# Kernel optimization log

Hardware: AMD Instinct MI355X
Metric: run time of the kernel (lower is better)

The kernel has to match this reference:

```python
import jax, jax.numpy as jnp
import numpy as np

EMBED_DIM = 1024
NUM_HEADS = 16
HEAD_DIM = EMBED_DIM // NUM_HEADS  # used only for the softmax scale


def setup_inputs() -> dict:
    key = jax.random.key(0)
    k_x, k_wqkv, k_bqkv, k_wo, k_bo = jax.random.split(key, 5)
    bound_qkv = 1.0 / np.sqrt(EMBED_DIM)
    return {
        "x": jax.random.normal(k_x, (4, 2048, EMBED_DIM), dtype=jnp.float32),
        "W_qkv": jax.random.uniform(k_wqkv, (EMBED_DIM, 3 * EMBED_DIM), jnp.float32, -bound_qkv, bound_qkv),
        "b_qkv": jax.random.uniform(k_bqkv, (3 * EMBED_DIM,), jnp.float32, -bound_qkv, bound_qkv),
        "W_out": jax.random.uniform(k_wo, (EMBED_DIM, EMBED_DIM), jnp.float32, -bound_qkv, bound_qkv),
        "b_out": jax.random.uniform(k_bo, (EMBED_DIM,), jnp.float32, -bound_qkv, bound_qkv),
    }


def reference(x, W_qkv, b_qkv, W_out, b_out):
    # fused QKV projection: [B,S,3E]
    qkv = jnp.einsum("bse,ef->bsf", x, W_qkv) + b_qkv
    q, k, v = jnp.split(qkv, 3, axis=-1)  # each [B,S,E]
    scale = 1.0 / jnp.sqrt(jnp.float32(HEAD_DIM))
    # NOTE: no head reshape — attention over full embed_dim, scale uses head_dim
    scores = jnp.einsum("bqe,bke->bqk", q, k) * scale  # [B,S,S]
    attn = jax.nn.softmax(scores, axis=-1)
    context = jnp.einsum("bqk,bke->bqe", attn, v)  # [B,S,E]
    return jnp.einsum("bse,ef->bsf", context, W_out) + b_out
```

## Files before the change

### kernel.cpp

```cpp
#include <hip/hip_runtime.h>

typedef unsigned short u16;
typedef __bf16   bf16x8 __attribute__((ext_vector_type(8)));
typedef float    f32x4  __attribute__((ext_vector_type(4)));
typedef unsigned short u16x4 __attribute__((ext_vector_type(4)));

__device__ inline float bf2f(u16 u) { return __uint_as_float(((unsigned int)u) << 16); }
__device__ inline u16 f2bf(float f) {
    unsigned int u = __float_as_uint(f);
    u += 0x7FFF + ((u >> 16) & 1);
    return (u16)(u >> 16);
}

__device__ inline void gl2lds16(const u16* g, u16* l) {
    __builtin_amdgcn_global_load_lds(
        (const __attribute__((address_space(1))) void*)g,
        (__attribute__((address_space(3))) void*)l, 16, 0, 0);
}

__global__ __launch_bounds__(256)
void sniff_zero(const u16* __restrict__ x, int* __restrict__ flag,
                float* __restrict__ sums) {
    sums[blockIdx.x * 256 + threadIdx.x] = 0.0f;
    if (blockIdx.x == 0 && threadIdx.x < 64) {
        const int lane = threadIdx.x;
        const unsigned idx = lane * 131072u + 65536u;
        const u16 u = x[idx];
        const int e = (u >> 7) & 0xFF;
        const unsigned long long b = __ballot(e >= 100 && e <= 140);
        if (lane == 0) flag[0] = (__popcll(b) >= 48) ? 0 : 1;
    }
}

__global__ __launch_bounds__(256)
void convx_biases(const void* __restrict__ x, u16* __restrict__ xbf,
                  const void* __restrict__ b1, const void* __restrict__ b2,
                  u16* __restrict__ o1, u16* __restrict__ o2,
                  const int* __restrict__ flagp) {
    const int f = *flagp;
    if (blockIdx.x < 8192) {
        const long i = ((long)blockIdx.x * 256 + threadIdx.x) * 4;
        if (f) {
            f32x4 v = *(const f32x4*)((const float*)x + i);
            u16x4 o; o[0] = f2bf(v[0]); o[1] = f2bf(v[1]); o[2] = f2bf(v[2]); o[3] = f2bf(v[3]);
            *(u16x4*)(xbf + i) = o;
        } else {
            *(u16x4*)(xbf + i) = *(const u16x4*)((const u16*)x + i);
        }
    } else {
        const int i = (blockIdx.x - 8192) * 256 + threadIdx.x;
        if (i < 3072) o1[i] = f ? f2bf(((const float*)b1)[i]) : ((const u16*)b1)[i];
        else { const int j = i - 3072;
               o2[j] = f ? f2bf(((const float*)b2)[j]) : ((const u16*)b2)[j]; }
    }
}

__global__ __launch_bounds__(256)
void transpose_w(const void* __restrict__ Wqkv, u16* __restrict__ WqkvT,
                 const void* __restrict__ Wout, u16* __restrict__ WoutT,
                 const int* __restrict__ flagp)
{
    const void* in; u16* out; long inStride, outStride;
    if (blockIdx.z == 0) { in = Wqkv; out = WqkvT; inStride = 3072; outStride = 1024; }
    else { if (blockIdx.x >= 32) return;
           in = Wout; out = WoutT; inStride = 1024; outStride = 1024; }
    __shared__ u16 t[32][36];
    const int isF32 = *flagp;
    const int tid = threadIdx.x;
    const long r0 = (long)blockIdx.y * 32;
    const long c0 = (long)blockIdx.x * 32;
    const int r  = tid >> 3;
    const int c4 = (tid & 7) * 4;
    const long base = (r0 + r) * inStride + c0 + c4;
    u16x4 v;
    if (isF32) {
        f32x4 f = *(const f32x4*)((const float*)in + base);
        v[0] = f2bf(f[0]); v[1] = f2bf(f[1]); v[2] = f2bf(f[2]); v[3] = f2bf(f[3]);
    } else {
        v = *(const u16x4*)((const u16*)in + base);
    }
    t[r][c4 + 0] = v[0]; t[r][c4 + 1] = v[1]; t[r][c4 + 2] = v[2]; t[r][c4 + 3] = v[3];
    __syncthreads();
    u16x4 o;
    o[0] = t[c4 + 0][r]; o[1] = t[c4 + 1][r]; o[2] = t[c4 + 2][r]; o[3] = t[c4 + 3][r];
    *(u16x4*)&out[(c0 + r) * outStride + r0 + c4] = o;
}

template <int GM, int GN, int WM, int WN, int EPI, int OUT_MODE, bool HAS_BIAS>
__global__ __launch_bounds__(256, 4)
void gemm_t(const u16* __restrict__ A, const u16* __restrict__ Bt,
            void* __restrict__ Cv, const u16* __restrict__ bias,
            int K, long lda, long ldb, long ldc,
            long aBatch, long bBatch, long cBatch, float scale,
            const int* __restrict__ flagp, float* __restrict__ sums)
{
    constexpr int BM = GM * WM * 16;
    constexpr int BN = GN * WN * 16;
    constexpr int IA = BM / 32;
    constexpr int IB = BN / 32;
    __shared__ __align__(16) u16 As[BM * 64];
    __shared__ __align__(16) u16 Bs[BN * 64];

    const int outF32 = (OUT_MODE == 2) ? *flagp : OUT_MODE;

    const int tid  = threadIdx.x;
    const int lane = tid & 63;
    const int wave = tid >> 6;
    const long m0 = (long)blockIdx.y * BM;
    const long n0 = (long)blockIdx.x * BN;
    const long bz = blockIdx.z;

    const int sr  = tid >> 3;
    const int qg0 = (tid & 7) ^ (sr & 7);
    const u16* pa[IA];
    const u16* pb[IB];
    u16* la[IA];
    u16* lb[IB];
#pragma unroll
    for (int i = 0; i < IA; ++i) {
        pa[i] = A + bz * aBatch + (m0 + i * 32 + sr) * lda + qg0 * 8;
        la[i] = As + (i * 256 + wave * 64) * 8;
    }
#pragma unroll
    for (int i = 0; i < IB; ++i) {
        pb[i] = Bt + bz * bBatch + (n0 + i * 32 + sr) * ldb + qg0 * 8;
        lb[i] = Bs + (i * 256 + wave * 64) * 8;
    }

    const int wm = (wave / GN) * (WM * 16);
    const int wn = (wave % GN) * (WN * 16);
    const int lr = lane & 15;
    const int hk = lane >> 4;

    int aoff[WM][2], boff[WN][2];
#pragma unroll
    for (int i = 0; i < WM; ++i) {
        const int row = wm + i * 16 + lr, r7 = row & 7;
        aoff[i][0] = row * 64 + ((hk     ^ r7) * 8);
        aoff[i][1] = row * 64 + (((4+hk) ^ r7) * 8);
    }
#pragma unroll
    for (int j = 0; j < WN; ++j) {
        const int row = wn + j * 16 + lr, r7 = row & 7;
        boff[j][0] = row * 64 + ((hk     ^ r7) * 8);
        boff[j][1] = row * 64 + (((4+hk) ^ r7) * 8);
    }

    f32x4 acc[WM][WN] = {};

    for (int kt = 0; kt < K; kt += 64) {
#pragma unroll
        for (int i = 0; i < IA; ++i) { gl2lds16(pa[i], la[i]); pa[i] += 64; }
#pragma unroll
        for (int i = 0; i < IB; ++i) { gl2lds16(pb[i], lb[i]); pb[i] += 64; }
        __syncthreads();

#pragma unroll
        for (int ks = 0; ks < 2; ++ks) {
            bf16x8 af[WM], bf[WN];
#pragma unroll
            for (int i = 0; i < WM; ++i) af[i] = *(const bf16x8*)&As[aoff[i][ks]];
#pragma unroll
            for (int j = 0; j < WN; ++j) bf[j] = *(const bf16x8*)&Bs[boff[j][ks]];
#pragma unroll
            for (int i = 0; i < WM; ++i)
#pragma unroll
                for (int j = 0; j < WN; ++j)
                    acc[i][j] = __builtin_amdgcn_mfma_f32_16x16x32_bf16(af[i], bf[j], acc[i][j], 0, 0, 0);
        }
        __syncthreads();
    }

    if (EPI == 1) {
#pragma unroll
        for (int i = 0; i < WM; ++i) {
#pragma unroll
            for (int r = 0; r < 4; ++r) {
                const long row = m0 + wm + i*16 + hk*4 + r;
                float s = 0.0f;
#pragma unroll
                for (int j = 0; j < WN; ++j) {
                    const long c = n0 + wn + j*16 + lr;
                    const float e = __expf(acc[i][j][r] * scale);
                    ((u16*)Cv)[bz * cBatch + row * ldc + c] = f2bf(e);
                    s += e;
                }
                s += __shfl_xor(s, 1); s += __shfl_xor(s, 2);
                s += __shfl_xor(s, 4); s += __shfl_xor(s, 8);
                if (lr == 0) atomicAdd(&sums[bz * 2048 + row], s);
            }
        }
    } else {
        float inv[WM][4];
        if (EPI == 2) {
#pragma unroll
            for (int i = 0; i < WM; ++i)
#pragma unroll
                for (int r = 0; r < 4; ++r)
                    inv[i][r] = 1.0f / sums[bz * 2048 + m0 + wm + i*16 + hk*4 + r];
        }
#pragma unroll
        for (int j = 0; j < WN; ++j) {
            const long c = n0 + wn + j*16 + lr;
            const float bj = HAS_BIAS ? bf2f(bias[c]) : 0.0f;
#pragma unroll
            for (int i = 0; i < WM; ++i) {
                const long rbase = m0 + wm + i*16 + hk * 4;
#pragma unroll
                for (int r = 0; r < 4; ++r) {
                    float v = (EPI == 2) ? acc[i][j][r] * inv[i][r] + bj
                                         : acc[i][j][r] * scale + bj;
                    const long ci = bz * cBatch + (rbase + r) * ldc + c;
                    if (outF32) ((float*)Cv)[ci] = v;
                    else        ((u16*)Cv)[ci]   = f2bf(v);
                }
            }
        }
    }
}

extern "C" void kernel_launch(void* const* d_in, const int* in_sizes, int n_in,
                              void* d_out, int out_size, void* d_ws, size_t ws_size,
                              hipStream_t stream)
{
    const void* x    = d_in[0];
    const void* Wqkv = d_in[1];
    const void* bqkv = d_in[2];
    const void* Wout = d_in[3];
    const void* bout = d_in[4];
    char* ws = (char*)d_ws;

    u16*   xbf   = (u16*)(ws);
    u16*   WqkvT = (u16*)(ws + 16777216);
    u16*   P     = (u16*)(ws);
    u16*   QKV   = (u16*)(ws + 33554432);
    u16*   VWT   = (u16*)(ws + 83886080);
    u16*   WoutT = (u16*)(ws + 100663296);
    u16*   bqkvc = (u16*)(ws + 102760448);
    u16*   boutc = (u16*)(ws + 102766592);
    int*   flag  = (int*)(ws + 102768640);
    float* sums  = (float*)(ws + 102772736);

    dim3 blk(256);

    sniff_zero<<<32, blk, 0, stream>>>((const u16*)x, flag, sums);
    convx_biases<<<8208, blk, 0, stream>>>(x, xbf, bqkv, bout, bqkvc, boutc, flag);
    transpose_w<<<dim3(96, 32, 2), blk, 0, stream>>>(Wqkv, WqkvT, Wout, WoutT, flag);

    gemm_t<2, 2, 4, 4, 0, 0, true><<<dim3(24, 64, 1), blk, 0, stream>>>(
        xbf, WqkvT, QKV, bqkvc, 1024, 1024L, 1024L, 3072L,
        0L, 0L, 0L, 1.0f, nullptr, nullptr);

    gemm_t<2, 2, 4, 4, 0, 0, false><<<dim3(16, 8, 4), blk, 0, stream>>>(
        WoutT, QKV + 2048, VWT, nullptr, 1024, 1024L, 3072L, 2048L,
        0L, 2048L * 3072L, 1024L * 2048L, 1.0f, nullptr, nullptr);

    gemm_t<2, 2, 4, 4, 1, 0, false><<<dim3(16, 16, 4), blk, 0, stream>>>(
        QKV, QKV + 1024, P, nullptr, 1024, 3072L, 3072L, 2048L,
        2048L * 3072L, 2048L * 3072L, 2048L * 2048L, 0.125f, nullptr, sums);

    gemm_t<2, 2, 4, 4, 2, 2, true><<<dim3(8, 16, 4), blk, 0, stream>>>(
        P, VWT, d_out, boutc, 2048, 2048L, 2048L, 1024L,
        2048L * 2048L, 1024L * 2048L, 2048L * 1024L, 1.0f, flag, sums);
}
```

Before: 276.3 us.

## Stage GEMM epilogues through LDS for vectorized stores; merge VW and QK GEMM launches

Each GEMM epilogue now writes accumulator tiles into per-wave LDS scratch (reusing the A/B tile buffers) and then writes them to global memory as 16-byte vector stores, replacing the scattered 2- and 4-byte per-element stores. The V·W_out projection and the QK^T/exp GEMM are combined into one launch, using blockIdx.z to pick the work, which removes one kernel launch and lets both fill the GPU together. The cost is extra LDS round trips and waitcnt stalls in the epilogue, plus branchy per-block dispatch in the merged kernel.

```diff
diff --git a/kernel.cpp b/kernel.cpp
--- a/kernel.cpp
+++ b/kernel.cpp
@@ -4,6 +4,7 @@
 typedef __bf16   bf16x8 __attribute__((ext_vector_type(8)));
 typedef float    f32x4  __attribute__((ext_vector_type(4)));
 typedef unsigned short u16x4 __attribute__((ext_vector_type(4)));
+typedef unsigned short u16x8 __attribute__((ext_vector_type(8)));
 
 __device__ inline float bf2f(u16 u) { return __uint_as_float(((unsigned int)u) << 16); }
 __device__ inline u16 f2bf(float f) {
@@ -86,52 +87,37 @@
     *(u16x4*)&out[(c0 + r) * outStride + r0 + c4] = o;
 }
 
-template <int GM, int GN, int WM, int WN, int EPI, int OUT_MODE, bool HAS_BIAS>
-__global__ __launch_bounds__(256, 4)
-void gemm_t(const u16* __restrict__ A, const u16* __restrict__ Bt,
-            void* __restrict__ Cv, const u16* __restrict__ bias,
-            int K, long lda, long ldb, long ldc,
-            long aBatch, long bBatch, long cBatch, float scale,
-            const int* __restrict__ flagp, float* __restrict__ sums)
+template <int GM, int GN, int WM, int WN>
+__device__ __forceinline__ void kloop(
+    const u16* __restrict__ A, const u16* __restrict__ Bt,
+    int K, long lda, long ldb, long m0, long n0,
+    u16* __restrict__ As, u16* __restrict__ Bs, f32x4 (&acc)[WM][WN])
 {
     constexpr int BM = GM * WM * 16;
     constexpr int BN = GN * WN * 16;
     constexpr int IA = BM / 32;
     constexpr int IB = BN / 32;
-    __shared__ __align__(16) u16 As[BM * 64];
-    __shared__ __align__(16) u16 Bs[BN * 64];
-
-    const int outF32 = (OUT_MODE == 2) ? *flagp : OUT_MODE;
-
     const int tid  = threadIdx.x;
     const int lane = tid & 63;
     const int wave = tid >> 6;
-    const long m0 = (long)blockIdx.y * BM;
-    const long n0 = (long)blockIdx.x * BN;
-    const long bz = blockIdx.z;
-
-    const int sr  = tid >> 3;
-    const int qg0 = (tid & 7) ^ (sr & 7);
-    const u16* pa[IA];
-    const u16* pb[IB];
-    u16* la[IA];
-    u16* lb[IB];
+    const int sr   = tid >> 3;
+    const int qg0  = (tid & 7) ^ (sr & 7);
+    const u16* pa[IA]; const u16* pb[IB];
+    u16* la[IA]; u16* lb[IB];
 #pragma unroll
     for (int i = 0; i < IA; ++i) {
-        pa[i] = A + bz * aBatch + (m0 + i * 32 + sr) * lda + qg0 * 8;
+        pa[i] = A + (m0 + i * 32 + sr) * lda + qg0 * 8;
         la[i] = As + (i * 256 + wave * 64) * 8;
     }
 #pragma unroll
     for (int i = 0; i < IB; ++i) {
-        pb[i] = Bt + bz * bBatch + (n0 + i * 32 + sr) * ldb + qg0 * 8;
+        pb[i] = Bt + (n0 + i * 32 + sr) * ldb + qg0 * 8;
         lb[i] = Bs + (i * 256 + wave * 64) * 8;
     }
-
     const int wm = (wave / GN) * (WM * 16);
     const int wn = (wave % GN) * (WN * 16);
     const int lr = lane & 15;
     const int hk = lane >> 4;
-
     int aoff[WM][2], boff[WN][2];
 #pragma unroll
     for (int i = 0; i < WM; ++i) {
@@ -145,16 +131,12 @@
         boff[j][0] = row * 64 + ((hk     ^ r7) * 8);
         boff[j][1] = row * 64 + (((4+hk) ^ r7) * 8);
     }
-
-    f32x4 acc[WM][WN] = {};
-
     for (int kt = 0; kt < K; kt += 64) {
 #pragma unroll
         for (int i = 0; i < IA; ++i) { gl2lds16(pa[i], la[i]); pa[i] += 64; }
 #pragma unroll
         for (int i = 0; i < IB; ++i) { gl2lds16(pb[i], lb[i]); pb[i] += 64; }
         __syncthreads();
-
 #pragma unroll
         for (int ks = 0; ks < 2; ++ks) {
             bf16x8 af[WM], bf[WN];
@@ -170,52 +152,170 @@
         }
         __syncthreads();
     }
-
-    if (EPI == 1) {
-#pragma unroll
-        for (int i = 0; i < WM; ++i) {
+}
+
+template <int WM, int WN, typename F>
+__device__ __forceinline__ void epi_bf16(u16* __restrict__ Sw, u16* __restrict__ C,
+    long ldc, long gm0, long gn0, int lane, F f)
+{
+    const int lr = lane & 15, hk = lane >> 4;
+#pragma unroll
+    for (int i = 0; i < WM; ++i)
+#pragma unroll
+        for (int j = 0; j < WN; ++j)
+#pragma unroll
+            for (int r = 0; r < 4; ++r)
+                Sw[(i*16 + hk*4 + r) * (WN*16) + j*16 + lr] = f2bf(f(i, j, r));
+    asm volatile("s_waitcnt lgkmcnt(0)" ::: "memory");
+    constexpr int LPR = WN * 2;
+    constexpr int RPI = 64 / LPR;
+    const int rl = lane / LPR, c8 = (lane % LPR) * 8;
+#pragma unroll
+    for (int t = 0; t < (WM*16) / RPI; ++t) {
+        const int row = t * RPI + rl;
+        u16x8 v8 = *(const u16x8*)&Sw[row * (WN*16) + c8];
+        *(u16x8*)&C[(gm0 + row) * ldc + gn0 + c8] = v8;
+    }
+}
+
+template <int WM, int WN, typename F>
+__device__ __forceinline__ void epi_f32(float* __restrict__ Sw, float* __restrict__ C,
+    long ldc, long gm0, long gn0, int lane, F f)
+{
+    const int lr = lane & 15, hk = lane >> 4;
+#pragma unroll
+    for (int jh = 0; jh < 2; ++jh) {
+#pragma unroll
+        for (int i = 0; i < WM; ++i)
+#pragma unroll
+            for (int jj = 0; jj < WN/2; ++jj)
+#pragma unroll
+                for (int r = 0; r < 4; ++r)
+                    Sw[(i*16 + hk*4 + r) * (WN*8) + jj*16 + lr] = f(i, jh*(WN/2) + jj, r);
+        asm volatile("s_waitcnt lgkmcnt(0)" ::: "memory");
+        constexpr int LPR = WN * 2;
+        constexpr int RPI = 64 / LPR;
+        const int rl = lane / LPR, c4 = (lane % LPR) * 4;
+#pragma unroll
+        for (int t = 0; t < (WM*16) / RPI; ++t) {
+            const int row = t * RPI + rl;
+            f32x4 v4 = *(const f32x4*)&Sw[row * (WN*8) + c4];
+            *(f32x4*)&C[(gm0 + row) * ldc + gn0 + jh*(WN*8) + c4] = v4;
+        }
+        asm volatile("s_waitcnt lgkmcnt(0)" ::: "memory");
+    }
+}
+
+__global__ __launch_bounds__(256, 4)
+void gemm_qkv(const u16* __restrict__ A, const u16* __restrict__ Bt,
+              u16* __restrict__ C, const u16* __restrict__ bias)
+{
+    __shared__ __align__(16) u16 S[256 * 64];
+    const long m0 = (long)blockIdx.y * 128, n0 = (long)blockIdx.x * 128;
+    f32x4 acc[4][4] = {};
+    kloop<2, 2, 4, 4>(A, Bt, 1024, 1024L, 1024L, m0, n0, S, S + 128*64, acc);
+    const int lane = threadIdx.x & 63, wave = threadIdx.x >> 6;
+    const int wm = (wave >> 1) * 64, wn = (wave & 1) * 64;
+    const int lr = lane & 15;
+    float bj[4];
+#pragma unroll
+    for (int j = 0; j < 4; ++j) bj[j] = bf2f(bias[n0 + wn + j*16 + lr]);
+    epi_bf16<4, 4>(S + wave * 4096, C, 3072L, m0 + wm, n0 + wn, lane,
+        [&](int i, int j, int r) { return acc[i][j][r] + bj[j]; });
+}
+
+__global__ __launch_bounds__(256, 4)
+void gemm_phase2(const u16* __restrict__ QKV, u16* __restrict__ P,
+                 const u16* __restrict__ WoutT, u16* __restrict__ VWT,
+                 float* __restrict__ sums)
+{
+    __shared__ __align__(16) u16 S[256 * 64];
+    const int z = blockIdx.z;
+    const u16 *Ap, *Bp; u16* Cp; long lda, ldb, ldc, m0, n0;
+    bool doExp; float* srow = nullptr;
+    if (z < 4) {
+        const long zb = (long)z * 2048 * 3072;
+        Ap = QKV + zb; Bp = QKV + 1024 + zb;
+        Cp = P + (long)z * 2048 * 2048;
+        lda = 3072; ldb = 3072; ldc = 2048;
+        m0 = (long)blockIdx.y * 128; n0 = (long)blockIdx.x * 128;
+        doExp = true; srow = sums + z * 2048;
+    } else {
+        const int vb = (z - 4) * 2 + (blockIdx.y >> 3);
+        Ap = WoutT; lda = 1024;
+        Bp = QKV + 2048 + (long)vb * 2048 * 3072; ldb = 3072;
+        Cp = VWT + (long)vb * 1024 * 2048; ldc = 2048;
+        m0 = (long)(blockIdx.y & 7) * 128; n0 = (long)blockIdx.x * 128;
+        doExp = false;
+    }
+    f32x4 acc[4][4] = {};
+    kloop<2, 2, 4, 4>(Ap, Bp, 1024, lda, ldb, m0, n0, S, S + 128*64, acc);
+    const int lane = threadIdx.x & 63, wave = threadIdx.x >> 6;
+    const int wm = (wave >> 1) * 64, wn = (wave & 1) * 64;
+    const int lr = lane & 15, hk = lane >> 4;
+    u16* Sw = S + wave * 4096;
+    if (doExp) {
+#pragma unroll
+        for (int i = 0; i < 4; ++i)
 #pragma unroll
             for (int r = 0; r < 4; ++r) {
-                const long row = m0 + wm + i*16 + hk*4 + r;
+                const int lrow = i*16 + hk*4 + r;
                 float s = 0.0f;
 #pragma unroll
-                for (int j = 0; j < WN; ++j) {
-                    const long c = n0 + wn + j*16 + lr;
-                    const float e = __expf(acc[i][j][r] * scale);
-                    ((u16*)Cv)[bz * cBatch + row * ldc + c] = f2bf(e);
+                for (int j = 0; j < 4; ++j) {
+                    const float e = __expf(acc[i][j][r] * 0.125f);
+                    Sw[lrow * 64 + j*16 + lr] = f2bf(e);
                     s += e;
                 }
                 s += __shfl_xor(s, 1); s += __shfl_xor(s, 2);
                 s += __shfl_xor(s, 4); s += __shfl_xor(s, 8);
-                if (lr == 0) atomicAdd(&sums[bz * 2048 + row], s);
+                if (lr == 0) atomicAdd(&srow[m0 + wm + lrow], s);
             }
+        asm volatile("s_waitcnt lgkmcnt(0)" ::: "memory");
+        const int rl = lane >> 3, c8 = (lane & 7) * 8;
+#pragma unroll
+        for (int t = 0; t < 8; ++t) {
+            const int row = t * 8 + rl;
+            u16x8 v8 = *(const u16x8*)&Sw[row * 64 + c8];
+            *(u16x8*)&Cp[(m0 + wm + row) * ldc + n0 + wn + c8] = v8;
         }
     } else {
-        float inv[WM][4];
-        if (EPI == 2) {
-#pragma unroll
-            for (int i = 0; i < WM; ++i)
-#pragma unroll
-                for (int r = 0; r < 4; ++r)
-                    inv[i][r] = 1.0f / sums[bz * 2048 + m0 + wm + i*16 + hk*4 + r];
-        }
-#pragma unroll
-        for (int j = 0; j < WN; ++j) {
-            const long c = n0 + wn + j*16 + lr;
-            const float bj = HAS_BIAS ? bf2f(bias[c]) : 0.0f;
-#pragma unroll
-            for (int i = 0; i < WM; ++i) {
-                const long rbase = m0 + wm + i*16 + hk * 4;
-#pragma unroll
-                for (int r = 0; r < 4; ++r) {
-                    float v = (EPI == 2) ? acc[i][j][r] * inv[i][r] + bj
-                                         : acc[i][j][r] * scale + bj;
-                    const long ci = bz * cBatch + (rbase + r) * ldc + c;
-                    if (outF32) ((float*)Cv)[ci] = v;
-                    else        ((u16*)Cv)[ci]   = f2bf(v);
-                }
-            }
-        }
+        epi_bf16<4, 4>(Sw, Cp, ldc, m0 + wm, n0 + wn, lane,
+            [&](int i, int j, int r) { return acc[i][j][r]; });
+    }
+}
+
+__global__ __launch_bounds__(256, 4)
+void gemm_final(const u16* __restrict__ P, const u16* __restrict__ VWT,
+                void* __restrict__ out, const u16* __restrict__ bias,
+                const float* __restrict__ sums, const int* __restrict__ flagp)
+{
+    __shared__ __align__(16) u16 S[256 * 64];
+    const int outF32 = *flagp;
+    const long bz = blockIdx.z;
+    const long m0 = (long)blockIdx.y * 128, n0 = (long)blockIdx.x * 128;
+    f32x4 acc[4][4] = {};
+    kloop<2, 2, 4, 4>(P + bz * 2048 * 2048, VWT + bz * 1024 * 2048,
+                      2048, 2048L, 2048L, m0, n0, S, S + 128*64, acc);
+    const int lane = threadIdx.x & 63, wave = threadIdx.x >> 6;
+    const int wm = (wave >> 1) * 64, wn = (wave & 1) * 64;
+    const int lr = lane & 15, hk = lane >> 4;
+    float inv[4][4], bj[4];
+#pragma unroll
+    for (int i = 0; i < 4; ++i)
+#pragma unroll
+        for (int r = 0; r < 4; ++r)
+            inv[i][r] = 1.0f / sums[bz * 2048 + m0 + wm + i*16 + hk*4 + r];
+#pragma unroll
+    for (int j = 0; j < 4; ++j) bj[j] = bf2f(bias[n0 + wn + j*16 + lr]);
+    if (outF32) {
+        float* Co = (float*)out + bz * 2048 * 1024;
+        epi_f32<4, 4>((float*)S + wave * 2048, Co, 1024L, m0 + wm, n0 + wn, lane,
+            [&](int i, int j, int r) { return acc[i][j][r] * inv[i][r] + bj[j]; });
+    } else {
+        u16* Co = (u16*)out + bz * 2048 * 1024;
+        epi_bf16<4, 4>(S + wave * 4096, Co, 1024L, m0 + wm, n0 + wn, lane,
+            [&](int i, int j, int r) { return acc[i][j][r] * inv[i][r] + bj[j]; });
     }
 }
 
@@ -247,19 +347,9 @@
     convx_biases<<<8208, blk, 0, stream>>>(x, xbf, bqkv, bout, bqkvc, boutc, flag);
     transpose_w<<<dim3(96, 32, 2), blk, 0, stream>>>(Wqkv, WqkvT, Wout, WoutT, flag);
 
-    gemm_t<2, 2, 4, 4, 0, 0, true><<<dim3(24, 64, 1), blk, 0, stream>>>(
-        xbf, WqkvT, QKV, bqkvc, 1024, 1024L, 1024L, 3072L,
-        0L, 0L, 0L, 1.0f, nullptr, nullptr);
-
-    gemm_t<2, 2, 4, 4, 0, 0, false><<<dim3(16, 8, 4), blk, 0, stream>>>(
-        WoutT, QKV + 2048, VWT, nullptr, 1024, 1024L, 3072L, 2048L,
-        0L, 2048L * 3072L, 1024L * 2048L, 1.0f, nullptr, nullptr);
-
-    gemm_t<2, 2, 4, 4, 1, 0, false><<<dim3(16, 16, 4), blk, 0, stream>>>(
-        QKV, QKV + 1024, P, nullptr, 1024, 3072L, 3072L, 2048L,
-        2048L * 3072L, 2048L * 3072L, 2048L * 2048L, 0.125f, nullptr, sums);
-
-    gemm_t<2, 2, 4, 4, 2, 2, true><<<dim3(8, 16, 4), blk, 0, stream>>>(
-        P, VWT, d_out, boutc, 2048, 2048L, 2048L, 1024L,
-        2048L * 2048L, 1024L * 2048L, 2048L * 1024L, 1.0f, flag, sums);
-}
+    gemm_qkv<<<dim3(24, 64, 1), blk, 0, stream>>>(xbf, WqkvT, QKV, bqkvc);
+
+    gemm_phase2<<<dim3(16, 16, 6), blk, 0, stream>>>(QKV, P, WoutT, VWT, sums);
+
+    gemm_final<<<dim3(8, 16, 4), blk, 0, stream>>>(P, VWT, d_out, boutc, sums, flag);
+}
```

Result: faster. 261.7 us (-5.3%).
